# Optimization experiments

Measured on AMD Instinct MI355X. Metric: run time of the kernel, lower is better.

## Reference

```python
import jax, jax.numpy as jnp
import numpy as np


def setup_inputs() -> dict:
    key = jax.random.key(0)
    k1, k2, k3, k4 = jax.random.split(key, 4)
    B, C, N, K, OUT = 2, 64, 50000, 9, 64
    x = jax.random.normal(k1, (B, C, N, 1), dtype=jnp.float32)
    edge_index = jax.random.randint(k2, (2, B, N, K), 0, N, dtype=jnp.int64)
    W1 = jax.random.normal(k3, (C, C), dtype=jnp.float32) * (1.0 / np.sqrt(C))
    b1 = jnp.zeros((C,), dtype=jnp.float32)
    W2 = jax.random.normal(k4, (OUT, 2 * C), dtype=jnp.float32) * (1.0 / np.sqrt(2 * C))
    b2 = jnp.zeros((OUT,), dtype=jnp.float32)
    return {"x": x, "edge_index": edge_index, "W1": W1, "b1": b1, "W2": W2, "b2": b2}


def _gather_neighbors(x_sq, idx):
    # x_sq: [B, C, N], idx: [B, N, K] -> [B, C, N, K]
    B, C, N = x_sq.shape
    K = idx.shape[-1]
    flat = jax.vmap(lambda xb, ib: xb[:, ib])(x_sq, idx.reshape(B, N * K))
    return flat.reshape(B, C, N, K)


def reference(x, edge_index, W1, b1, W2, b2):
    # x: [B, C, N, 1]; edge_index[0]: [B, N, K] neighbor indices
    x_sq = x[..., 0]                                   # [B, C, N]
    x_j = _gather_neighbors(x_sq, edge_index[0])       # [B, C, N, K]
    # nn1: 1x1 conv (per-node linear over channels) + ReLU
    h = jax.nn.relu(jnp.einsum('bcnk,dc->bdnk', x_j, W1) + b1[None, :, None, None])
    x_j_max = jnp.max(h, axis=-1, keepdims=True)       # [B, C, N, 1]
    cat = jnp.concatenate([x, x_j_max], axis=1)        # [B, 2C, N, 1]
    # nn2: 1x1 conv + ReLU
    out = jax.nn.relu(jnp.einsum('bcnk,dc->bdnk', cat, W2) + b2[None, :, None, None])
    return out                                          # [B, OUT, N, 1]
```

## Files before the change

### kernel.cpp

```cpp
#include <hip/hip_runtime.h>
#include <cstddef>

typedef unsigned int uint;
typedef _Float16 v8h __attribute__((ext_vector_type(8)));
typedef float v4f __attribute__((ext_vector_type(4)));
typedef __fp16 fp16v2 __attribute__((ext_vector_type(2)));
typedef unsigned short us2v __attribute__((ext_vector_type(2)));

union U32H2 { uint u; fp16v2 g; us2v s; };
union Frag8 { uint4 u4; uint u[4]; v8h h; };

__device__ __forceinline__ uint pkh2(float a, float b) {
  U32H2 v; v.g = __builtin_amdgcn_cvt_pkrtz(a, b); return v.u;
}
__device__ __forceinline__ uint hmax2u(uint a, uint b) {
  U32H2 x, y, r; x.u = a; y.u = b;
  r.s = __builtin_elementwise_max(x.s, y.s);
  return r.u;
}

__global__ __launch_bounds__(256, 4) void k1_node_mlp(
    const float* __restrict__ x, const float* __restrict__ W1,
    const float* __restrict__ b1, uint* __restrict__ y, int N)
{
  __shared__ __align__(16) uint xlds[64 * 36];
  __shared__ __align__(16) uint ylds[64 * 34];
  const int t = threadIdx.x;
  const int nblk = (N + 63) >> 6;
  const int b = blockIdx.x / nblk;
  const int n0 = (blockIdx.x % nblk) << 6;
  const int lane = t & 63;
  const int w = t >> 6;
  const int node = t >> 2;
  const int cg = t & 3;

  {
    const bool valid = (n0 + node) < N;
    const float* xp = x + (size_t)b * 64 * N + n0 + node;
    float xv[16];
#pragma unroll
    for (int i = 0; i < 16; ++i)
      xv[i] = valid ? xp[(size_t)(cg * 16 + i) * N] : 0.0f;
    uint4 p0, p1;
    p0.x = pkh2(xv[0], xv[1]);   p0.y = pkh2(xv[2], xv[3]);
    p0.z = pkh2(xv[4], xv[5]);   p0.w = pkh2(xv[6], xv[7]);
    p1.x = pkh2(xv[8], xv[9]);   p1.y = pkh2(xv[10], xv[11]);
    p1.z = pkh2(xv[12], xv[13]); p1.w = pkh2(xv[14], xv[15]);
    uint* dst = xlds + node * 36 + cg * 8;
    *(uint4*)dst = p0;
    *(uint4*)(dst + 4) = p1;
  }

  Frag8 af[2];
  {
    const int d_row = w * 16 + (lane & 15);
    const int kb = (lane >> 4) * 8;
    const float* wp = W1 + d_row * 64 + kb;
#pragma unroll
    for (int kk = 0; kk < 2; ++kk) {
      const float4 fa = *(const float4*)(wp + kk * 32);
      const float4 fb = *(const float4*)(wp + kk * 32 + 4);
      af[kk].u4.x = pkh2(fa.x, fa.y);
      af[kk].u4.y = pkh2(fa.z, fa.w);
      af[kk].u4.z = pkh2(fb.x, fb.y);
      af[kk].u4.w = pkh2(fb.z, fb.w);
    }
  }
  __syncthreads();

  const int q = lane >> 4;
  const int cidx = lane & 15;
  const int d0 = w * 16;
  v4f acc[4];
  {
    v4f bi;
#pragma unroll
    for (int r = 0; r < 4; ++r) bi[r] = b1[d0 + q * 4 + r];
#pragma unroll
    for (int nt = 0; nt < 4; ++nt) acc[nt] = bi;
  }
#pragma unroll
  for (int nt = 0; nt < 4; ++nt) {
#pragma unroll
    for (int kk = 0; kk < 2; ++kk) {
      Frag8 bf;
      bf.u4 = *(const uint4*)(xlds + (nt * 16 + cidx) * 36 + kk * 16 + q * 4);
      acc[nt] = __builtin_amdgcn_mfma_f32_16x16x32_f16(af[kk].h, bf.h, acc[nt], 0, 0, 0);
    }
  }

#pragma unroll
  for (int nt = 0; nt < 4; ++nt) {
    const int nn = nt * 16 + cidx;
    const uint p01 = pkh2(fmaxf(acc[nt][0], 0.f), fmaxf(acc[nt][1], 0.f));
    const uint p23 = pkh2(fmaxf(acc[nt][2], 0.f), fmaxf(acc[nt][3], 0.f));
    ylds[nn * 34 + (d0 >> 1) + 2 * q] = p01;
    ylds[nn * 34 + (d0 >> 1) + 2 * q + 1] = p23;
  }
  __syncthreads();
#pragma unroll
  for (int p = 0; p < 4; ++p) {
    const int f = t + (p << 8);
    const int nn = f >> 4, ch = f & 15;
    if (n0 + nn < N) {
      const uint2 v = *(const uint2*)(ylds + nn * 34 + ch * 2);
      *(uint2*)(y + ((size_t)b * N + n0 + nn) * 32 + ch * 2) = v;
    }
  }
}

__global__ __launch_bounds__(256, 4) void k2_gather_out(
    const float* __restrict__ x, const int* __restrict__ eidx,
    const uint* __restrict__ y, const float* __restrict__ W2,
    const float* __restrict__ b2, float* __restrict__ out, int N, int K)
{
  __shared__ __align__(16) uint blds[64 * 68];
  const int t = threadIdx.x;
  const int nblk = (N + 63) >> 6;
  const int b = blockIdx.x / nblk;
  const int n0 = (blockIdx.x % nblk) << 6;
  const int lane = t & 63;
  const int w = t >> 6;
  const int node = t >> 2;
  const int cg = t & 3;
  const int n = n0 + node;

  const bool is64 = (__ballot(eidx[2 * lane + 1] == 0) == ~0ull);

  int jj[9];
  const bool act = (n < N) && (K == 9);
  if (act) {
    const size_t r = (size_t)b * N + n;
    if (is64) {
      const uint2* p = (const uint2*)eidx + r * 9;
#pragma unroll
      for (int k = 0; k < 9; ++k) jj[k] = (int)p[k].x;
    } else {
      const int* p = eidx + r * 9;
#pragma unroll
      for (int k = 0; k < 9; ++k) jj[k] = p[k];
    }
  }

  {
    const bool valid = n < N;
    const float* xp = x + (size_t)b * 64 * N + n0 + node;
    float xv[16];
#pragma unroll
    for (int i = 0; i < 16; ++i)
      xv[i] = valid ? xp[(size_t)(cg * 16 + i) * N] : 0.0f;
    uint4 p0, p1;
    p0.x = pkh2(xv[0], xv[1]);   p0.y = pkh2(xv[2], xv[3]);
    p0.z = pkh2(xv[4], xv[5]);   p0.w = pkh2(xv[6], xv[7]);
    p1.x = pkh2(xv[8], xv[9]);   p1.y = pkh2(xv[10], xv[11]);
    p1.z = pkh2(xv[12], xv[13]); p1.w = pkh2(xv[14], xv[15]);
    uint* dst = blds + node * 68 + cg * 8;
    *(uint4*)dst = p0;
    *(uint4*)(dst + 4) = p1;
  }

  Frag8 af[4];
  {
    const int o_row = w * 16 + (lane & 15);
    const int kb = (lane >> 4) * 8;
    const float* wp = W2 + o_row * 128 + kb;
#pragma unroll
    for (int kk = 0; kk < 4; ++kk) {
      const float4 fa = *(const float4*)(wp + kk * 32);
      const float4 fb = *(const float4*)(wp + kk * 32 + 4);
      af[kk].u4.x = pkh2(fa.x, fa.y);
      af[kk].u4.y = pkh2(fa.z, fa.w);
      af[kk].u4.z = pkh2(fb.x, fb.y);
      af[kk].u4.w = pkh2(fb.z, fb.w);
    }
  }

  uint m[8] = {0, 0, 0, 0, 0, 0, 0, 0};
  if (act) {
    const uint* yb = y + (size_t)b * N * 32 + cg * 8;
    uint4 g[10];
#pragma unroll
    for (int k = 0; k < 5; ++k) {
      const uint* base = yb + (size_t)jj[k] * 32;
      g[2 * k] = *(const uint4*)base;
      g[2 * k + 1] = *(const uint4*)(base + 4);
    }
#pragma unroll
    for (int k = 0; k < 5; ++k) {
      m[0] = hmax2u(m[0], g[2 * k].x); m[1] = hmax2u(m[1], g[2 * k].y);
      m[2] = hmax2u(m[2], g[2 * k].z); m[3] = hmax2u(m[3], g[2 * k].w);
      m[4] = hmax2u(m[4], g[2 * k + 1].x); m[5] = hmax2u(m[5], g[2 * k + 1].y);
      m[6] = hmax2u(m[6], g[2 * k + 1].z); m[7] = hmax2u(m[7], g[2 * k + 1].w);
    }
#pragma unroll
    for (int k = 0; k < 4; ++k) {
      const uint* base = yb + (size_t)jj[5 + k] * 32;
      g[2 * k] = *(const uint4*)base;
      g[2 * k + 1] = *(const uint4*)(base + 4);
    }
#pragma unroll
    for (int k = 0; k < 4; ++k) {
      m[0] = hmax2u(m[0], g[2 * k].x); m[1] = hmax2u(m[1], g[2 * k].y);
      m[2] = hmax2u(m[2], g[2 * k].z); m[3] = hmax2u(m[3], g[2 * k].w);
      m[4] = hmax2u(m[4], g[2 * k + 1].x); m[5] = hmax2u(m[5], g[2 * k + 1].y);
      m[6] = hmax2u(m[6], g[2 * k + 1].z); m[7] = hmax2u(m[7], g[2 * k + 1].w);
    }
  } else if (n < N) {
    const size_t r = (size_t)b * N + n;
    const uint* yb = y + (size_t)b * N * 32 + cg * 8;
    for (int k = 0; k < K; ++k) {
      const int j = is64 ? (int)((const uint2*)eidx + r * K)[k].x
                         : (eidx + r * K)[k];
      const uint* base = yb + (size_t)j * 32;
      const uint4 a0 = *(const uint4*)base, a1 = *(const uint4*)(base + 4);
      m[0] = hmax2u(m[0], a0.x); m[1] = hmax2u(m[1], a0.y);
      m[2] = hmax2u(m[2], a0.z); m[3] = hmax2u(m[3], a0.w);
      m[4] = hmax2u(m[4], a1.x); m[5] = hmax2u(m[5], a1.y);
      m[6] = hmax2u(m[6], a1.z); m[7] = hmax2u(m[7], a1.w);
    }
  }
  {
    uint* dst = blds + node * 68 + 32 + cg * 8;
    uint4 v0; v0.x = m[0]; v0.y = m[1]; v0.z = m[2]; v0.w = m[3];
    uint4 v1; v1.x = m[4]; v1.y = m[5]; v1.z = m[6]; v1.w = m[7];
    *(uint4*)dst = v0;
    *(uint4*)(dst + 4) = v1;
  }
  __syncthreads();

  const int q = lane >> 4;
  const int cidx = lane & 15;
  const int o0 = w * 16;
  v4f acc[4];
  {
    v4f bi;
#pragma unroll
    for (int r = 0; r < 4; ++r) bi[r] = b2[o0 + q * 4 + r];
#pragma unroll
    for (int nt = 0; nt < 4; ++nt) acc[nt] = bi;
  }
#pragma unroll
  for (int nt = 0; nt < 4; ++nt) {
#pragma unroll
    for (int kk = 0; kk < 4; ++kk) {
      Frag8 bf;
      bf.u4 = *(const uint4*)(blds + (nt * 16 + cidx) * 68 + kk * 16 + q * 4);
      acc[nt] = __builtin_amdgcn_mfma_f32_16x16x32_f16(af[kk].h, bf.h, acc[nt], 0, 0, 0);
    }
  }

#pragma unroll
  for (int nt = 0; nt < 4; ++nt) {
    const int nn = n0 + nt * 16 + cidx;
    if (nn < N) {
#pragma unroll
      for (int r = 0; r < 4; ++r) {
        const int o = o0 + q * 4 + r;
        out[(size_t)(b * 64 + o) * N + nn] = fmaxf(acc[nt][r], 0.f);
      }
    }
  }
}

extern "C" void kernel_launch(void* const* d_in, const int* in_sizes, int n_in,
                              void* d_out, int out_size, void* d_ws, size_t ws_size,
                              hipStream_t stream) {
  const float* x  = (const float*)d_in[0];
  const int*   ei = (const int*)d_in[1];
  const float* W1 = (const float*)d_in[2];
  const float* b1 = (const float*)d_in[3];
  const float* W2 = (const float*)d_in[4];
  const float* b2 = (const float*)d_in[5];
  float* out = (float*)d_out;

  const int N = in_sizes[0] / 128;
  const int K = in_sizes[1] / (4 * N);

  uint* y = (uint*)d_ws;

  const int nblk = (N + 63) >> 6;
  k1_node_mlp<<<2 * nblk, 256, 0, stream>>>(x, W1, b1, y, N);
  k2_gather_out<<<2 * nblk, 256, 0, stream>>>(x, ei, y, W2, b2, out, N, K);
}
```

Measured before the change: 116.9 us.

## Drop LDS staging in node MLP, remap gather blocks, issue all neighbor loads at once

The node-MLP kernel now writes its packed fp16 outputs straight from MFMA registers to global memory instead of staging them through LDS. That removes one shared buffer and a barrier, and the occupancy hint is raised. The gather kernel interleaves block indices so that blocks for both batches and adjacent tiles run together, and it pads the grid to a multiple of four with early exit for out-of-range tiles. All nine neighbor row loads are issued before the max reduction, which gives more memory-level parallelism at the cost of more registers.

```diff
diff --git a/kernel.cpp b/kernel.cpp
--- a/kernel.cpp
+++ b/kernel.cpp
@@ -19,12 +19,11 @@
   return r.u;
 }
 
-__global__ __launch_bounds__(256, 4) void k1_node_mlp(
+__global__ __launch_bounds__(256, 6) void k1_node_mlp(
     const float* __restrict__ x, const float* __restrict__ W1,
     const float* __restrict__ b1, uint* __restrict__ y, int N)
 {
   __shared__ __align__(16) uint xlds[64 * 36];
-  __shared__ __align__(16) uint ylds[64 * 34];
   const int t = threadIdx.x;
   const int nblk = (N + 63) >> 6;
   const int b = blockIdx.x / nblk;
@@ -70,12 +69,11 @@
 
   const int q = lane >> 4;
   const int cidx = lane & 15;
-  const int d0 = w * 16;
   v4f acc[4];
   {
     v4f bi;
 #pragma unroll
-    for (int r = 0; r < 4; ++r) bi[r] = b1[d0 + q * 4 + r];
+    for (int r = 0; r < 4; ++r) bi[r] = b1[w * 16 + q * 4 + r];
 #pragma unroll
     for (int nt = 0; nt < 4; ++nt) acc[nt] = bi;
   }
@@ -91,20 +89,12 @@
 
 #pragma unroll
   for (int nt = 0; nt < 4; ++nt) {
-    const int nn = nt * 16 + cidx;
-    const uint p01 = pkh2(fmaxf(acc[nt][0], 0.f), fmaxf(acc[nt][1], 0.f));
-    const uint p23 = pkh2(fmaxf(acc[nt][2], 0.f), fmaxf(acc[nt][3], 0.f));
-    ylds[nn * 34 + (d0 >> 1) + 2 * q] = p01;
-    ylds[nn * 34 + (d0 >> 1) + 2 * q + 1] = p23;
-  }
-  __syncthreads();
-#pragma unroll
-  for (int p = 0; p < 4; ++p) {
-    const int f = t + (p << 8);
-    const int nn = f >> 4, ch = f & 15;
-    if (n0 + nn < N) {
-      const uint2 v = *(const uint2*)(ylds + nn * 34 + ch * 2);
-      *(uint2*)(y + ((size_t)b * N + n0 + nn) * 32 + ch * 2) = v;
+    const int n = n0 + nt * 16 + cidx;
+    if (n < N) {
+      uint2 v;
+      v.x = pkh2(fmaxf(acc[nt][0], 0.f), fmaxf(acc[nt][1], 0.f));
+      v.y = pkh2(fmaxf(acc[nt][2], 0.f), fmaxf(acc[nt][3], 0.f));
+      *(uint2*)(y + ((size_t)b * N + n) * 32 + w * 8 + q * 2) = v;
     }
   }
 }
@@ -112,13 +102,18 @@
 __global__ __launch_bounds__(256, 4) void k2_gather_out(
     const float* __restrict__ x, const int* __restrict__ eidx,
     const uint* __restrict__ y, const float* __restrict__ W2,
-    const float* __restrict__ b2, float* __restrict__ out, int N, int K)
+    const float* __restrict__ b2, float* __restrict__ out,
+    int N, int K, int nblk_pad)
 {
   __shared__ __align__(16) uint blds[64 * 68];
   const int t = threadIdx.x;
   const int nblk = (N + 63) >> 6;
-  const int b = blockIdx.x / nblk;
-  const int n0 = (blockIdx.x % nblk) << 6;
+  const int g = blockIdx.x;
+  const int slot = g & 7;
+  const int b = slot >> 2;
+  const int tile = ((g >> 3) << 2) + (slot & 3);
+  if (tile >= nblk) return;
+  const int n0 = tile << 6;
   const int lane = t & 63;
   const int w = t >> 6;
   const int node = t >> 2;
@@ -178,32 +173,19 @@
   uint m[8] = {0, 0, 0, 0, 0, 0, 0, 0};
   if (act) {
     const uint* yb = y + (size_t)b * N * 32 + cg * 8;
-    uint4 g[10];
-#pragma unroll
-    for (int k = 0; k < 5; ++k) {
+    uint4 ga[9], gb[9];
+#pragma unroll
+    for (int k = 0; k < 9; ++k) {
       const uint* base = yb + (size_t)jj[k] * 32;
-      g[2 * k] = *(const uint4*)base;
-      g[2 * k + 1] = *(const uint4*)(base + 4);
-    }
-#pragma unroll
-    for (int k = 0; k < 5; ++k) {
-      m[0] = hmax2u(m[0], g[2 * k].x); m[1] = hmax2u(m[1], g[2 * k].y);
-      m[2] = hmax2u(m[2], g[2 * k].z); m[3] = hmax2u(m[3], g[2 * k].w);
-      m[4] = hmax2u(m[4], g[2 * k + 1].x); m[5] = hmax2u(m[5], g[2 * k + 1].y);
-      m[6] = hmax2u(m[6], g[2 * k + 1].z); m[7] = hmax2u(m[7], g[2 * k + 1].w);
-    }
-#pragma unroll
-    for (int k = 0; k < 4; ++k) {
-      const uint* base = yb + (size_t)jj[5 + k] * 32;
-      g[2 * k] = *(const uint4*)base;
-      g[2 * k + 1] = *(const uint4*)(base + 4);
-    }
-#pragma unroll
-    for (int k = 0; k < 4; ++k) {
-      m[0] = hmax2u(m[0], g[2 * k].x); m[1] = hmax2u(m[1], g[2 * k].y);
-      m[2] = hmax2u(m[2], g[2 * k].z); m[3] = hmax2u(m[3], g[2 * k].w);
-      m[4] = hmax2u(m[4], g[2 * k + 1].x); m[5] = hmax2u(m[5], g[2 * k + 1].y);
-      m[6] = hmax2u(m[6], g[2 * k + 1].z); m[7] = hmax2u(m[7], g[2 * k + 1].w);
+      ga[k] = *(const uint4*)base;
+      gb[k] = *(const uint4*)(base + 4);
+    }
+#pragma unroll
+    for (int k = 0; k < 9; ++k) {
+      m[0] = hmax2u(m[0], ga[k].x); m[1] = hmax2u(m[1], ga[k].y);
+      m[2] = hmax2u(m[2], ga[k].z); m[3] = hmax2u(m[3], ga[k].w);
+      m[4] = hmax2u(m[4], gb[k].x); m[5] = hmax2u(m[5], gb[k].y);
+      m[6] = hmax2u(m[6], gb[k].z); m[7] = hmax2u(m[7], gb[k].w);
     }
   } else if (n < N) {
     const size_t r = (size_t)b * N + n;
@@ -279,6 +261,7 @@
   uint* y = (uint*)d_ws;
 
   const int nblk = (N + 63) >> 6;
+  const int nblk_pad = (nblk + 3) & ~3;
   k1_node_mlp<<<2 * nblk, 256, 0, stream>>>(x, W1, b1, y, N);
-  k2_gather_out<<<2 * nblk, 256, 0, stream>>>(x, ei, y, W2, b2, out, N, K);
-}
+  k2_gather_out<<<2 * nblk_pad, 256, 0, stream>>>(x, ei, y, W2, b2, out, N, K, nblk_pad);
+}
```

Result: no change. 119.1 us (+1.8%).
